# Kernel optimization log

Measured on AMD Instinct MI355X. Metric: run time of the kernel, lower is better.

## Reference

```python
import jax, jax.numpy as jnp
import numpy as np

TRIM = 0.2
ALPHA = 0.5
SCALES = 4
B, H, W = 64, 384, 512


def _normalize_robust(x, mask):
    # per-sample masked median shift, masked mean-abs-dev scale (MiDaS SSI norm)
    b = x.shape[0]
    xf = x.reshape(b, -1)
    mf = mask.reshape(b, -1)
    n = mf.sum(axis=1)                                   # valid count per row
    s = jnp.sort(jnp.where(mf, xf, jnp.inf), axis=1)     # masked-out -> +inf, sorted to tail
    med_idx = jnp.maximum((n - 1) // 2, 0)               # torch.median = lower median
    shift = jnp.take_along_axis(s, med_idx[:, None], axis=1)      # [b,1]
    scale = (jnp.abs(xf - shift) * mf).sum(axis=1) / n.astype(xf.dtype)
    return ((xf - shift) / scale[:, None]).reshape(x.shape)


def _gradient_loss(pred, targ):
    mask = targ > 0
    gx = jnp.abs(pred[:, :, 1:] - pred[:, :, :-1])
    gy = jnp.abs(pred[:, 1:, :] - pred[:, :-1, :])
    mx = (mask[:, :, 1:] & mask[:, :, :-1]).astype(pred.dtype)
    my = (mask[:, 1:, :] & mask[:, :-1, :]).astype(pred.dtype)
    norm = mask.sum(axis=(1, 2))
    loss = (gx * mx).sum(axis=(1, 2)) + (gy * my).sum(axis=(1, 2))
    valid = norm > 0
    loss = jnp.where(valid, loss / jnp.maximum(norm, 1).astype(pred.dtype), 0.0)
    return loss.mean()


def _multiscale_gradient_loss(pred, targ):
    total = jnp.asarray(0.0, pred.dtype)
    for scale in range(SCALES):
        step = 2 ** scale
        total = total + _gradient_loss(pred[:, ::step, ::step], targ[:, ::step, ::step])
    return total


def _trimmed_mae(pred, targ):
    b = pred.shape[0]
    p = pred.reshape(b, -1)
    t = targ.reshape(b, -1)
    n_px = p.shape[1]
    mask = t > 0
    res = jnp.where(mask, jnp.abs(p - t), 0.0)
    # NOTE: faithful to source, which indexes the UNSORTED res at max_index
    # (sorted_res is computed then never used for the threshold).
    max_index = (~mask).sum(axis=1) + int((1.0 - TRIM) * n_px)
    max_index = jnp.minimum(max_index, n_px - 1)
    thr = jnp.take_along_axis(res, max_index[:, None], axis=1)    # [b,1]
    res = jnp.where(res > thr, 0.0, res)
    norm = 2 * mask.sum(axis=1)
    valid = norm > 0
    loss = res.sum(axis=1)
    loss = jnp.where(valid, loss / jnp.maximum(norm, 1).astype(p.dtype), 0.0)
    return loss.mean()


def setup_inputs() -> dict:
    key = jax.random.key(0)
    kp, kt = jax.random.split(key)
    prediction = jax.random.normal(kp, (B, H, W), dtype=jnp.float32)
    target = jax.random.normal(kt, (B, H, W), dtype=jnp.float32)
    return {"prediction": prediction, "target": target}


def reference(prediction, target):
    mask = target > 0
    pred_n = _normalize_robust(prediction, mask)
    targ_n = _normalize_robust(target, mask)
    loss = _trimmed_mae(pred_n, targ_n)
    loss = loss + ALPHA * _multiscale_gradient_loss(pred_n, targ_n)
    return loss
```

## Files before the change

kernel.cpp:

```cpp
#include <hip/hip_runtime.h>
#include <stdint.h>

#define B 64
#define H 384
#define W 512
#define NPX (H*W)
#define TRIM_IDX 157286
#define RPW 8

#define NBA 2048
#define CAPW 256
#define NSLOT 64
#define CAPD 12288
#define SCAP 6144
#define DELTA 0.03f

#define N_OFF    0
#define MS_OFF   64
#define TS_OFF   256
#define GS_OFF   320
#define TSUM_OFF 576
#define SB_OFF   704
#define CB_OFF   832
#define OVF_OFF  960
#define ZERO_U32 1088
#define BL_OFF   1088
#define BH_OFF   1216
#define K_OFF    1344
#define EQ_OFF   1472
#define SH_OFF   1600
#define RS_OFF   1728
#define THR_OFF  1856
#define C2_OFF   1920
#define CNTW_OFF 1984
#define FIX_U32  (1984 + 2*B*NSLOT)
#define BUF_OFF  FIX_U32

__device__ __forceinline__ uint32_t fmap(float f) {
    uint32_t b = __float_as_uint(f);
    return (b & 0x80000000u) ? ~b : (b | 0x80000000u);
}
__device__ __forceinline__ float funmap(uint32_t u) {
    uint32_t b = (u & 0x80000000u) ? (u & 0x7fffffffu) : ~u;
    return __uint_as_float(b);
}

__global__ void __launch_bounds__(1024) sample_kernel(const float* __restrict__ pred,
                                                      const float* __restrict__ targ,
                                                      uint32_t* __restrict__ ws) {
    __shared__ uint32_t kp[SCAP], kt[SCAP];
    __shared__ uint32_t h[4096];
    __shared__ uint32_t sc[256];
    __shared__ uint32_t s_ct, s_lo12, s_hi12, s_clo, s_bl, s_bh;
    const int b = blockIdx.x;
    const int t = threadIdx.x;
    const int lane = t & 63;
    if (t == 0) s_ct = 0;
    __syncthreads();
    const float4* pb = (const float4*)(pred + (size_t)b * NPX);
    const float4* tb = (const float4*)(targ + (size_t)b * NPX);
    #pragma unroll
    for (int c = 0; c < 2; c++) {
        int j = t + c * 1024;
        int q = ((j >> 6) * 1536) + (j & 63);
        float4 tv = tb[q], pv = pb[q];
        float tA[4] = {tv.x, tv.y, tv.z, tv.w};
        float pA[4] = {pv.x, pv.y, pv.z, pv.w};
        #pragma unroll
        for (int e = 0; e < 4; e++) {
            bool msk = tA[e] > 0.f;
            unsigned long long bal = __ballot(msk);
            if (bal) {
                int leader = __ffsll((long long)bal) - 1;
                uint32_t base = 0;
                if (lane == leader) base = atomicAdd(&s_ct, (uint32_t)__popcll(bal));
                base = (uint32_t)__shfl((int)base, leader, 64);
                if (msk) {
                    uint32_t off = base + (uint32_t)__popcll(bal & ((1ull << lane) - 1ull));
                    if (off < SCAP) { kt[off] = fmap(tA[e]); kp[off] = fmap(pA[e]); }
                }
            }
        }
    }
    __syncthreads();
    const uint32_t ct = s_ct;
    const bool ok = (ct > 0) && (ct <= SCAP);
    for (int w = 0; w < 2; w++) {
        const uint32_t* K = (w == 0) ? kp : kt;
        uint32_t BL = 0, BH = 0xFFFFFu;
        if (ok) {
            uint32_t rlo = (uint32_t)((0.5f - DELTA) * (float)ct);
            uint32_t rhi = (uint32_t)((0.5f + DELTA) * (float)ct);
            if (rhi >= ct) rhi = ct - 1;
            for (int i = t; i < 4096; i += 1024) h[i] = 0;
            __syncthreads();
            for (uint32_t j = t; j < ct; j += 1024) atomicAdd(&h[K[j] >> 20], 1u);
            __syncthreads();
            uint32_t ms = 0;
            if (t < 256) { for (int i = 0; i < 16; i++) ms += h[t * 16 + i]; sc[t] = ms; }
            __syncthreads();
            for (int off = 1; off < 256; off <<= 1) {
                uint32_t a = (t < 256 && t >= off) ? sc[t - off] : 0u;
                __syncthreads();
                if (t < 256) sc[t] += a;
                __syncthreads();
            }
            if (t < 256) {
                uint32_t incl = sc[t], excl = incl - ms;
                if (rlo >= excl && rlo < incl) {
                    uint32_t c2 = excl;
                    for (int i = 0; i < 16; i++) {
                        uint32_t hv = h[t * 16 + i];
                        if (rlo < c2 + hv) { s_lo12 = t * 16 + i; s_clo = c2; break; }
                        c2 += hv;
                    }
                }
                if (rhi >= excl && rhi < incl) {
                    uint32_t c2 = excl;
                    for (int i = 0; i < 16; i++) {
                        uint32_t hv = h[t * 16 + i];
                        if (rhi < c2 + hv) { s_hi12 = t * 16 + i; break; }
                        c2 += hv;
                    }
                }
            }
            __syncthreads();
            const uint32_t lo12 = s_lo12, hi12 = s_hi12, clo = s_clo;
            const uint32_t range = (hi12 - lo12 + 1) << 8;
            if (range > 4096) {
                BL = lo12 << 8; BH = (hi12 << 8) | 255u;
            } else {
                for (int i = t; i < 4096; i += 1024) h[i] = 0;
                __syncthreads();
                const uint32_t base20 = lo12 << 8;
                for (uint32_t j = t; j < ct; j += 1024) {
                    uint32_t u = K[j], u12 = u >> 20;
                    if (u12 >= lo12 && u12 <= hi12) atomicAdd(&h[(u >> 12) - base20], 1u);
                }
                __syncthreads();
                const uint32_t r2lo = rlo - clo, r2hi = rhi - clo;
                uint32_t ms2 = 0;
                if (t < 256) { for (int i = 0; i < 16; i++) ms2 += h[t * 16 + i]; sc[t] = ms2; }
                __syncthreads();
                for (int off = 1; off < 256; off <<= 1) {
                    uint32_t a = (t < 256 && t >= off) ? sc[t - off] : 0u;
                    __syncthreads();
                    if (t < 256) sc[t] += a;
                    __syncthreads();
                }
                if (t < 256) {
                    uint32_t incl = sc[t], excl = incl - ms2;
                    if (r2lo >= excl && r2lo < incl) {
                        uint32_t c2 = excl;
                        for (int i = 0; i < 16; i++) {
                            uint32_t hv = h[t * 16 + i];
                            if (r2lo < c2 + hv) { s_bl = base20 + t * 16 + i; break; }
                            c2 += hv;
                        }
                    }
                    if (r2hi >= excl && r2hi < incl) {
                        uint32_t c2 = excl;
                        for (int i = 0; i < 16; i++) {
                            uint32_t hv = h[t * 16 + i];
                            if (r2hi < c2 + hv) { s_bh = base20 + t * 16 + i; break; }
                            c2 += hv;
                        }
                    }
                }
                __syncthreads();
                BL = s_bl; BH = s_bh;
            }
        }
        if (t == 0) { ws[BL_OFF + w * B + b] = BL; ws[BH_OFF + w * B + b] = BH; }
        __syncthreads();
    }
}

__global__ void __launch_bounds__(256) collect_kernel(const float* __restrict__ pred,
                                                      const float* __restrict__ targ,
                                                      uint32_t* __restrict__ ws, int capw) {
    const int b = blockIdx.y;
    const int t = threadIdx.x;
    const int lane = t & 63;
    const int slot = (blockIdx.x << 2) + (t >> 6);
    const uint32_t BLp = ws[BL_OFF + b],     BHp = ws[BH_OFF + b];
    const uint32_t BLt = ws[BL_OFF + B + b], BHt = ws[BH_OFF + B + b];
    const float4* pb = (const float4*)(pred + (size_t)b * NPX);
    const float4* tb = (const float4*)(targ + (size_t)b * NPX);
    const int tid = blockIdx.x * 256 + t;
    float* bufp = ((float*)(ws + BUF_OFF)) + ((size_t)b * NSLOT + slot) * capw;
    float* buft = ((float*)(ws + BUF_OFF)) + (((size_t)B + b) * NSLOT + slot) * capw;
    float sbp = 0.f, sbt = 0.f, sump = 0.f, sumt = 0.f;
    uint32_t nloc = 0, cbp = 0, cbt = 0;
    uint32_t wp = 0, wt = 0;
    #pragma unroll
    for (int r = 0; r < 3; r++) {
        float4 ta0 = tb[tid + (4*r+0)*4096], ta1 = tb[tid + (4*r+1)*4096];
        float4 ta2 = tb[tid + (4*r+2)*4096], ta3 = tb[tid + (4*r+3)*4096];
        float4 pa0 = pb[tid + (4*r+0)*4096], pa1 = pb[tid + (4*r+1)*4096];
        float4 pa2 = pb[tid + (4*r+2)*4096], pa3 = pb[tid + (4*r+3)*4096];
        float tA[16] = {ta0.x,ta0.y,ta0.z,ta0.w, ta1.x,ta1.y,ta1.z,ta1.w,
                        ta2.x,ta2.y,ta2.z,ta2.w, ta3.x,ta3.y,ta3.z,ta3.w};
        float pA[16] = {pa0.x,pa0.y,pa0.z,pa0.w, pa1.x,pa1.y,pa1.z,pa1.w,
                        pa2.x,pa2.y,pa2.z,pa2.w, pa3.x,pa3.y,pa3.z,pa3.w};
        uint32_t mbp = 0, mbt = 0;
        #pragma unroll
        for (int e = 0; e < 16; e++) {
            float tv = tA[e], pv = pA[e];
            if (tv > 0.f) {
                nloc++; sumt += tv; sump += pv;
                uint32_t up = fmap(pv) >> 12, ut = fmap(tv) >> 12;
                if (up < BLp) { cbp++; sbp += pv; }
                else if (up <= BHp) mbp |= (1u << e);
                if (ut < BLt) { cbt++; sbt += tv; }
                else if (ut <= BHt) mbt |= (1u << e);
            }
        }
        uint32_t packed = (uint32_t)__popc(mbp) | ((uint32_t)__popc(mbt) << 16);
        uint32_t scan = packed;
        #pragma unroll
        for (int off = 1; off < 64; off <<= 1) {
            uint32_t v = (uint32_t)__shfl_up((int)scan, off, 64);
            if (lane >= off) scan += v;
        }
        uint32_t tot = (uint32_t)__shfl((int)scan, 63, 64);
        uint32_t exl = scan - packed;
        uint32_t op = wp + (exl & 0xFFFFu);
        uint32_t ot = wt + (exl >> 16);
        if (mbp | mbt) {
            #pragma unroll
            for (int e = 0; e < 16; e++) {
                if ((mbp >> e) & 1u) { if (op < (uint32_t)capw) bufp[op] = pA[e]; op++; }
                if ((mbt >> e) & 1u) { if (ot < (uint32_t)capw) buft[ot] = tA[e]; ot++; }
            }
        }
        wp += tot & 0xFFFFu;
        wt += tot >> 16;
    }
    if (lane == 0) {
        ws[CNTW_OFF + b * NSLOT + slot] = wp;
        ws[CNTW_OFF + (B + b) * NSLOT + slot] = wt;
        if (wp > (uint32_t)capw) ws[OVF_OFF + b] = 1u;
        if (wt > (uint32_t)capw) ws[OVF_OFF + B + b] = 1u;
    }
    for (int off = 32; off; off >>= 1) {
        nloc += __shfl_down(nloc, off, 64);
        sump += __shfl_down(sump, off, 64);
        sumt += __shfl_down(sumt, off, 64);
        sbp  += __shfl_down(sbp, off, 64);
        sbt  += __shfl_down(sbt, off, 64);
        cbp  += __shfl_down(cbp, off, 64);
        cbt  += __shfl_down(cbt, off, 64);
    }
    if (lane == 0) {
        if (nloc) atomicAdd(ws + N_OFF + b, nloc);
        atomicAdd(((float*)(ws + TSUM_OFF)) + b, sump);
        atomicAdd(((float*)(ws + TSUM_OFF)) + B + b, sumt);
        atomicAdd(((float*)(ws + SB_OFF)) + b, sbp);
        atomicAdd(((float*)(ws + SB_OFF)) + B + b, sbt);
        if (cbp) atomicAdd(ws + CB_OFF + b, cbp);
        if (cbt) atomicAdd(ws + CB_OFF + B + b, cbt);
    }
}

__global__ void small3_kernel(const float* __restrict__ pred,
                              const float* __restrict__ targ,
                              uint32_t* __restrict__ ws, int capw) {
    const int b = blockIdx.x, which = blockIdx.y;
    const int t = threadIdx.x;
    __shared__ float dense[CAPD];
    __shared__ uint32_t cnt[4096];
    __shared__ float fsm[4096];
    __shared__ uint32_t sc[256];
    __shared__ float sfl[256];
    __shared__ uint32_t scnt[NSLOT], soff[NSLOT];
    __shared__ uint32_t r_bin, r_k, s_Ctot;
    __shared__ float r_f, s_facc;
    const uint32_t n = ws[N_OFF + b];
    const uint32_t k0 = (n - 1u) >> 1;
    const uint32_t CBv = ws[CB_OFF + which * B + b];
    const uint32_t* cw = ws + CNTW_OFF + (which * B + b) * NSLOT;
    const float* bufb = ((const float*)(ws + BUF_OFF)) + ((size_t)which * B + b) * NSLOT * capw;
    const float* Tp = targ + (size_t)b * NPX;
    const float* Pp = pred + (size_t)b * NPX;

    uint32_t myc = (t < NSLOT) ? cw[t] : 0u;
    sc[t] = myc;
    __syncthreads();
    for (int off = 1; off < NSLOT; off <<= 1) {
        uint32_t a = (t >= off) ? sc[t - off] : 0u;
        __syncthreads();
        sc[t] += a;
        __syncthreads();
    }
    if (t < NSLOT) { scnt[t] = myc; soff[t] = sc[t] - myc; }
    if (t == NSLOT - 1) s_Ctot = sc[t];
    __syncthreads();
    const uint32_t Ctot = s_Ctot;
    const long k_in = (long)k0 - (long)CBv;
    const bool fast = (capw > 0) && (ws[OVF_OFF + which * B + b] == 0u) &&
                      (Ctot <= (uint32_t)CAPD) && (k_in >= 0) && (k_in < (long)Ctot);
    if (fast) {
        const int s = t >> 2;
        const float* sb_ = bufb + (size_t)s * capw;
        const uint32_t nn = scnt[s], o = soff[s];
        for (uint32_t j = (uint32_t)(t & 3); j < nn; j += 4) dense[o + j] = sb_[j];
    }
    __syncthreads();

    uint32_t kr = fast ? (uint32_t)k_in : k0;

    for (int i = t; i < 4096; i += 256) { cnt[i] = 0; fsm[i] = 0.f; }
    __syncthreads();
    if (fast) {
        for (uint32_t j = t; j < Ctot; j += 256) {
            float v = dense[j];
            uint32_t key = fmap(v) >> 20;
            atomicAdd(&cnt[key], 1u); atomicAdd(&fsm[key], v);
        }
    } else {
        for (int j = t; j < NPX; j += 256) {
            float tvv = Tp[j];
            if (tvv > 0.f) {
                float v = (which == 0) ? Pp[j] : tvv;
                uint32_t key = fmap(v) >> 20;
                atomicAdd(&cnt[key], 1u); atomicAdd(&fsm[key], v);
            }
        }
    }
    __syncthreads();
    {
        uint32_t ms = 0; float mf = 0.f;
        #pragma unroll
        for (int i = 0; i < 16; i++) { ms += cnt[t * 16 + i]; mf += fsm[t * 16 + i]; }
        sc[t] = ms; sfl[t] = mf;
        __syncthreads();
        for (int off = 1; off < 256; off <<= 1) {
            uint32_t a = (t >= off) ? sc[t - off] : 0u;
            float af = (t >= off) ? sfl[t - off] : 0.f;
            __syncthreads();
            sc[t] += a; sfl[t] += af;
            __syncthreads();
        }
        uint32_t incl = sc[t], excl = incl - ms;
        float fx = sfl[t] - mf;
        if (kr >= excl && kr < incl) {
            uint32_t c = excl, bin = 0, nk = 0; float f = fx;
            for (int i = 0; i < 16; i++) {
                uint32_t hv = cnt[t * 16 + i];
                if (kr < c + hv) { bin = t * 16 + i; nk = kr - c; break; }
                c += hv; f += fsm[t * 16 + i];
            }
            r_bin = bin; r_k = nk; r_f = f;
        }
    }
    __syncthreads();
    const uint32_t sel0 = r_bin;
    kr = r_k;
    if (t == 0) s_facc = r_f;
    __syncthreads();

    for (int i = t; i < NBA; i += 256) { cnt[i] = 0; fsm[i] = 0.f; }
    __syncthreads();
    if (fast) {
        for (uint32_t j = t; j < Ctot; j += 256) {
            float v = dense[j];
            uint32_t u = fmap(v);
            if ((u >> 20) == sel0) {
                uint32_t key = (u >> 9) & (NBA - 1u);
                atomicAdd(&cnt[key], 1u); atomicAdd(&fsm[key], v);
            }
        }
    } else {
        for (int j = t; j < NPX; j += 256) {
            float tvv = Tp[j];
            if (tvv > 0.f) {
                float v = (which == 0) ? Pp[j] : tvv;
                uint32_t u = fmap(v);
                if ((u >> 20) == sel0) {
                    uint32_t key = (u >> 9) & (NBA - 1u);
                    atomicAdd(&cnt[key], 1u); atomicAdd(&fsm[key], v);
                }
            }
        }
    }
    __syncthreads();
    {
        uint32_t ms = 0; float mf = 0.f;
        #pragma unroll
        for (int i = 0; i < 8; i++) { ms += cnt[t * 8 + i]; mf += fsm[t * 8 + i]; }
        sc[t] = ms; sfl[t] = mf;
        __syncthreads();
        for (int off = 1; off < 256; off <<= 1) {
            uint32_t a = (t >= off) ? sc[t - off] : 0u;
            float af = (t >= off) ? sfl[t - off] : 0.f;
            __syncthreads();
            sc[t] += a; sfl[t] += af;
            __syncthreads();
        }
        uint32_t incl = sc[t], excl = incl - ms;
        float fx = sfl[t] - mf;
        if (kr >= excl && kr < incl) {
            uint32_t c = excl, bin = 0, nk = 0; float f = fx;
            for (int i = 0; i < 8; i++) {
                uint32_t hv = cnt[t * 8 + i];
                if (kr < c + hv) { bin = t * 8 + i; nk = kr - c; break; }
                c += hv; f += fsm[t * 8 + i];
            }
            r_bin = bin; r_k = nk; r_f = f;
        }
    }
    __syncthreads();
    const uint32_t pfx23 = (sel0 << 11) | r_bin;
    kr = r_k;
    if (t == 0) s_facc += r_f;
    __syncthreads();

    for (int i = t; i < 512; i += 256) { cnt[i] = 0; fsm[i] = 0.f; }
    __syncthreads();
    if (fast) {
        for (uint32_t j = t; j < Ctot; j += 256) {
            float v = dense[j];
            uint32_t u = fmap(v);
            if ((u >> 9) == pfx23) {
                uint32_t key = u & 511u;
                atomicAdd(&cnt[key], 1u); atomicAdd(&fsm[key], v);
            }
        }
    } else {
        for (int j = t; j < NPX; j += 256) {
            float tvv = Tp[j];
            if (tvv > 0.f) {
                float v = (which == 0) ? Pp[j] : tvv;
                uint32_t u = fmap(v);
                if ((u >> 9) == pfx23) {
                    uint32_t key = u & 511u;
                    atomicAdd(&cnt[key], 1u); atomicAdd(&fsm[key], v);
                }
            }
        }
    }
    __syncthreads();
    {
        uint32_t ms = 0; float mf = 0.f;
        #pragma unroll
        for (int i = 0; i < 2; i++) { ms += cnt[t * 2 + i]; mf += fsm[t * 2 + i]; }
        sc[t] = ms; sfl[t] = mf;
        __syncthreads();
        for (int off = 1; off < 256; off <<= 1) {
            uint32_t a = (t >= off) ? sc[t - off] : 0u;
            float af = (t >= off) ? sfl[t - off] : 0.f;
            __syncthreads();
            sc[t] += a; sfl[t] += af;
            __syncthreads();
        }
        uint32_t incl = sc[t], excl = incl - ms;
        float fx = sfl[t] - mf;
        if (kr >= excl && kr < incl) {
            uint32_t c = excl, bin = 0, nk = 0, e = 0; float f = fx;
            for (int i = 0; i < 2; i++) {
                uint32_t hv = cnt[t * 2 + i];
                if (kr < c + hv) { bin = t * 2 + i; nk = kr - c; e = hv; break; }
                c += hv; f += fsm[t * 2 + i];
            }
            uint32_t u = (pfx23 << 9) | bin;
            ((float*)(ws + SH_OFF))[which * B + b] = funmap(u);
            ws[K_OFF + which * B + b] = nk;
            ws[EQ_OFF + which * B + b] = e;
            float* sb = ((float*)(ws + SB_OFF)) + which * B + b;
            float below = s_facc + f;
            *sb = fast ? (*sb + below) : below;
        }
    }
}

__global__ void param_kernel(const float* __restrict__ pred,
                             const float* __restrict__ targ,
                             uint32_t* __restrict__ ws) {
    const int b = threadIdx.x;
    if (b >= B) return;
    const uint32_t n = ws[N_OFF + b];
    const uint32_t k0 = (n - 1u) >> 1;
    float med[2], rs[2];
    uint32_t nab[2];
    #pragma unroll
    for (int w = 0; w < 2; w++) {
        float m = ((const float*)(ws + SH_OFF))[w * B + b];
        uint32_t k3 = ws[K_OFF + w * B + b];
        uint32_t e = ws[EQ_OFF + w * B + b];
        float SBv = ((const float*)(ws + SB_OFF))[w * B + b];
        float ST = ((const float*)(ws + TSUM_OFF))[w * B + b];
        uint32_t CB = k0 - k3;
        uint32_t na = n - CB - e;
        float Sab = ST - SBv - (float)e * m;
        float absdev = (Sab - (float)na * m) + ((float)CB * m - SBv);
        float scale = absdev / (float)n;
        med[w] = m; nab[w] = na;
        rs[w] = 1.f / scale;
        ((float*)(ws + RS_OFF))[w * B + b] = rs[w];
    }
    uint32_t c2 = nab[1];
    ws[C2_OFF + b] = c2;
    uint32_t mi = (uint32_t)NPX - c2 + (uint32_t)TRIM_IDX;
    if (mi > (uint32_t)(NPX - 1)) mi = NPX - 1;
    float p = pred[(size_t)b * NPX + mi];
    float t = targ[(size_t)b * NPX + mi];
    float pn = (p - med[0]) * rs[0], tn = (t - med[1]) * rs[1];
    ((float*)(ws + THR_OFF))[b] = (tn > 0.f) ? fabsf(pn - tn) : 0.f;
}

__global__ void __launch_bounds__(256) loss_kernel(const float* __restrict__ pred,
                                                   const float* __restrict__ targ,
                                                   uint32_t* __restrict__ ws) {
    const int wid = (blockIdx.x << 2) + (threadIdx.x >> 6);
    const int b = wid / (H / RPW);
    const int s0 = (wid - b * (H / RPW)) * RPW;
    const int l = threadIdx.x & 63;
    const int col = l << 3;
    const float sp = ((const float*)(ws + SH_OFF))[b];
    const float st = ((const float*)(ws + SH_OFF))[B + b];
    const float rp = ((const float*)(ws + RS_OFF))[b];
    const float rt = ((const float*)(ws + RS_OFF))[B + b];
    const float thr = ((const float*)(ws + THR_OFF))[b];
    const float* Pp = pred + (size_t)b * NPX;
    const float* Tp = targ + (size_t)b * NPX;

    const bool g1 = s0 >= 1, g2 = s0 >= 2, g4 = s0 >= 4, g8 = s0 >= 8;
    float rT[2][8], rPN[2][8];
    {
        const int roA = (g1 ? (s0 - 1) : s0) * W + col;
        const int roB = (g2 ? (s0 - 2) : s0) * W + col;
        float4 a0 = *(const float4*)(Tp + roA), a1 = *(const float4*)(Tp + roA + 4);
        float4 b0 = *(const float4*)(Pp + roA), b1 = *(const float4*)(Pp + roA + 4);
        float4 c0 = *(const float4*)(Tp + roB), c1 = *(const float4*)(Tp + roB + 4);
        float4 d0 = *(const float4*)(Pp + roB), d1 = *(const float4*)(Pp + roB + 4);
        float ta[8] = {a0.x,a0.y,a0.z,a0.w,a1.x,a1.y,a1.z,a1.w};
        float pa[8] = {b0.x,b0.y,b0.z,b0.w,b1.x,b1.y,b1.z,b1.w};
        float tc[8] = {c0.x,c0.y,c0.z,c0.w,c1.x,c1.y,c1.z,c1.w};
        float pc[8] = {d0.x,d0.y,d0.z,d0.w,d1.x,d1.y,d1.z,d1.w};
        #pragma unroll
        for (int k = 0; k < 8; k++) {
            rT[1][k] = ta[k]; rPN[1][k] = (pa[k] - sp) * rp;
            rT[0][k] = tc[k]; rPN[0][k] = (pc[k] - sp) * rp;
        }
    }

    float tl = 0.f, gl0 = 0.f, gl1 = 0.f, gl2 = 0.f, gl3 = 0.f;
    uint32_t mc = 0;

    #pragma unroll
    for (int it = 0; it < RPW; ++it) {
        const int ro = (s0 + it) * W + col;
        const int cur = it & 1, prv = cur ^ 1;
        float4 a0 = *(const float4*)(Tp + ro), a1 = *(const float4*)(Tp + ro + 4);
        float4 b0 = *(const float4*)(Pp + ro), b1 = *(const float4*)(Pp + ro + 4);
        float t[8] = {a0.x,a0.y,a0.z,a0.w,a1.x,a1.y,a1.z,a1.w};
        float p[8] = {b0.x,b0.y,b0.z,b0.w,b1.x,b1.y,b1.z,b1.w};
        float t4a = 0.f, t4b = 0.f, p4a = 0.f, p4b = 0.f, t8a = 0.f, p8a = 0.f;
        if (it == 0) {
            const int ro4 = g4 ? ro - 4 * W : ro;
            t4a = Tp[ro4]; t4b = Tp[ro4 + 4]; p4a = Pp[ro4]; p4b = Pp[ro4 + 4];
            const int ro8 = g8 ? ro - 8 * W : ro;
            t8a = Tp[ro8]; p8a = Pp[ro8];
        }
        if (it == 4) {
            const int ro4 = ro - 4 * W;
            t4a = Tp[ro4]; t4b = Tp[ro4 + 4]; p4a = Pp[ro4]; p4b = Pp[ro4 + 4];
        }
        float pn[8]; bool m[8];
        #pragma unroll
        for (int k = 0; k < 8; k++) { pn[k] = (p[k] - sp) * rp; m[k] = t[k] > st; }

        #pragma unroll
        for (int k = 0; k < 8; k++) {
            if (m[k]) {
                float tn = (t[k] - st) * rt;
                float r = fabsf(pn[k] - tn);
                if (r <= thr) tl += r;
            }
        }
        float t7p = __shfl_up(t[7], 1), pn7p = __shfl_up(pn[7], 1);
        if (l > 0 && m[0] && t7p > st) gl0 += fabsf(pn[0] - pn7p);
        #pragma unroll
        for (int k = 1; k < 8; k++) if (m[k] && m[k - 1]) gl0 += fabsf(pn[k] - pn[k - 1]);
        if (it > 0 || g1) {
            #pragma unroll
            for (int k = 0; k < 8; k++)
                if (m[k] && rT[prv][k] > st) gl0 += fabsf(pn[k] - rPN[prv][k]);
        }
        if ((it & 1) == 0) {
            float t6p = __shfl_up(t[6], 1), pn6p = __shfl_up(pn[6], 1);
            mc += (uint32_t)m[0] + m[2] + m[4] + m[6];
            if (l > 0 && m[0] && t6p > st) gl1 += fabsf(pn[0] - pn6p);
            if (m[2] && m[0]) gl1 += fabsf(pn[2] - pn[0]);
            if (m[4] && m[2]) gl1 += fabsf(pn[4] - pn[2]);
            if (m[6] && m[4]) gl1 += fabsf(pn[6] - pn[4]);
            if (it >= 2 || g2) {
                if (m[0] && rT[cur][0] > st) gl1 += fabsf(pn[0] - rPN[cur][0]);
                if (m[2] && rT[cur][2] > st) gl1 += fabsf(pn[2] - rPN[cur][2]);
                if (m[4] && rT[cur][4] > st) gl1 += fabsf(pn[4] - rPN[cur][4]);
                if (m[6] && rT[cur][6] > st) gl1 += fabsf(pn[6] - rPN[cur][6]);
            }
            if ((it & 3) == 0) {
                float t4p = __shfl_up(t[4], 1), pn4p = __shfl_up(pn[4], 1);
                mc += ((uint32_t)m[0] + m[4]) << 11;
                if (l > 0 && m[0] && t4p > st) gl2 += fabsf(pn[0] - pn4p);
                if (m[4] && m[0]) gl2 += fabsf(pn[4] - pn[0]);
                if (it == 4 || g4) {
                    if (m[0] && t4a > st) gl2 += fabsf(pn[0] - (p4a - sp) * rp);
                    if (m[4] && t4b > st) gl2 += fabsf(pn[4] - (p4b - sp) * rp);
                }
                if (it == 0) {
                    float t0p = __shfl_up(t[0], 1), pn0p = __shfl_up(pn[0], 1);
                    mc += ((uint32_t)m[0]) << 22;
                    if (l > 0 && m[0] && t0p > st) gl3 += fabsf(pn[0] - pn0p);
                    if (g8 && m[0] && t8a > st) gl3 += fabsf(pn[0] - (p8a - sp) * rp);
                }
            }
        }
        #pragma unroll
        for (int k = 0; k < 8; k++) { rT[cur][k] = t[k]; rPN[cur][k] = pn[k]; }
    }

    for (int off = 32; off; off >>= 1) {
        tl  += __shfl_down(tl, off, 64);
        gl0 += __shfl_down(gl0, off, 64);
        gl1 += __shfl_down(gl1, off, 64);
        gl2 += __shfl_down(gl2, off, 64);
        gl3 += __shfl_down(gl3, off, 64);
        mc  += __shfl_down(mc, off, 64);
    }
    if (l == 0) {
        float* gs = (float*)(ws + GS_OFF);
        atomicAdd(((float*)(ws + TS_OFF)) + b, tl);
        atomicAdd(gs + b, gl0);
        atomicAdd(gs + B + b, gl1);
        atomicAdd(gs + 2 * B + b, gl2);
        atomicAdd(gs + 3 * B + b, gl3);
        atomicAdd(ws + MS_OFF + b, mc & 0x7FFu);
        atomicAdd(ws + MS_OFF + B + b, (mc >> 11) & 0x7FFu);
        atomicAdd(ws + MS_OFF + 2 * B + b, mc >> 22);
    }
}

__global__ void finalize_kernel(const uint32_t* __restrict__ ws, float* __restrict__ out) {
    const int b = threadIdx.x;
    float v = 0.f;
    if (b < B) {
        float c2 = (float)ws[C2_OFF + b];
        const float* tsum = (const float*)(ws + TS_OFF);
        const float* gsum = (const float*)(ws + GS_OFF);
        float tm = (c2 > 0.f) ? tsum[b] / (2.f * c2) : 0.f;
        float g = (c2 > 0.f) ? gsum[b] / c2 : 0.f;
        for (int z = 0; z < 3; z++) {
            float ms = (float)ws[MS_OFF + z * B + b];
            g += (ms > 0.f) ? gsum[(1 + z) * B + b] / ms : 0.f;
        }
        v = tm + 0.5f * g;
    }
    for (int off = 32; off; off >>= 1) v += __shfl_down(v, off, 64);
    if (b == 0) out[0] = v * (1.f / 64.f);
}

extern "C" void kernel_launch(void* const* d_in, const int* in_sizes, int n_in,
                              void* d_out, int out_size, void* d_ws, size_t ws_size,
                              hipStream_t stream) {
    const float* pred = (const float*)d_in[0];
    const float* targ = (const float*)d_in[1];
    float* out = (float*)d_out;
    uint32_t* ws = (uint32_t*)d_ws;

    long avail = (long)(ws_size / 4) - (long)FIX_U32;
    int capw = 0;
    if (avail > 0) {
        long c = avail / (2L * B * NSLOT);
        capw = (int)(c < CAPW ? c : CAPW);
    }

    hipMemsetAsync(ws, 0, (size_t)ZERO_U32 * 4, stream);

    sample_kernel<<<dim3(B), 1024, 0, stream>>>(pred, targ, ws);
    collect_kernel<<<dim3(16, B), 256, 0, stream>>>(pred, targ, ws, capw);
    small3_kernel<<<dim3(B, 2), 256, 0, stream>>>(pred, targ, ws, capw);
    param_kernel<<<1, 64, 0, stream>>>(pred, targ, ws);
    loss_kernel<<<dim3(B * (H / RPW) / 4), 256, 0, stream>>>(pred, targ, ws);
    finalize_kernel<<<1, 64, 0, stream>>>(ws, out);
}
```

Baseline: 146.0 us.

## Remove memset and param kernel launches, fold params into loss kernel

Drops the workspace memset by zeroing the per-sample accumulators inside sample_kernel, and removes param_kernel by having each loss_kernel thread recompute median, scale and trim threshold from the workspace. It also changes collect_kernel so each block reads a contiguous chunk instead of a strided one. Together these remove two stream operations and improve locality. In exchange every loss thread does redundant scalar math plus a gather load for the threshold.

```diff
diff --git a/kernel.cpp b/kernel.cpp
--- a/kernel.cpp
+++ b/kernel.cpp
@@ -23,13 +23,11 @@
 #define SB_OFF   704
 #define CB_OFF   832
 #define OVF_OFF  960
-#define ZERO_U32 1088
 #define BL_OFF   1088
 #define BH_OFF   1216
 #define K_OFF    1344
 #define EQ_OFF   1472
 #define SH_OFF   1600
-#define RS_OFF   1728
 #define THR_OFF  1856
 #define C2_OFF   1920
 #define CNTW_OFF 1984
@@ -55,7 +53,21 @@
     const int b = blockIdx.x;
     const int t = threadIdx.x;
     const int lane = t & 63;
-    if (t == 0) s_ct = 0;
+    if (t == 0) {
+        s_ct = 0;
+        ws[N_OFF + b] = 0; ws[TS_OFF + b] = 0;
+        #pragma unroll
+        for (int z = 0; z < 3; z++) ws[MS_OFF + z * B + b] = 0;
+        #pragma unroll
+        for (int w2 = 0; w2 < 4; w2++) ws[GS_OFF + w2 * B + b] = 0;
+        #pragma unroll
+        for (int w2 = 0; w2 < 2; w2++) {
+            ws[TSUM_OFF + w2 * B + b] = 0;
+            ws[SB_OFF + w2 * B + b] = 0;
+            ws[CB_OFF + w2 * B + b] = 0;
+            ws[OVF_OFF + w2 * B + b] = 0;
+        }
+    }
     __syncthreads();
     const float4* pb = (const float4*)(pred + (size_t)b * NPX);
     const float4* tb = (const float4*)(targ + (size_t)b * NPX);
@@ -187,7 +199,7 @@
     const uint32_t BLt = ws[BL_OFF + B + b], BHt = ws[BH_OFF + B + b];
     const float4* pb = (const float4*)(pred + (size_t)b * NPX);
     const float4* tb = (const float4*)(targ + (size_t)b * NPX);
-    const int tid = blockIdx.x * 256 + t;
+    const int bbase = blockIdx.x * 3072;
     float* bufp = ((float*)(ws + BUF_OFF)) + ((size_t)b * NSLOT + slot) * capw;
     float* buft = ((float*)(ws + BUF_OFF)) + (((size_t)B + b) * NSLOT + slot) * capw;
     float sbp = 0.f, sbt = 0.f, sump = 0.f, sumt = 0.f;
@@ -195,10 +207,9 @@
     uint32_t wp = 0, wt = 0;
     #pragma unroll
     for (int r = 0; r < 3; r++) {
-        float4 ta0 = tb[tid + (4*r+0)*4096], ta1 = tb[tid + (4*r+1)*4096];
-        float4 ta2 = tb[tid + (4*r+2)*4096], ta3 = tb[tid + (4*r+3)*4096];
-        float4 pa0 = pb[tid + (4*r+0)*4096], pa1 = pb[tid + (4*r+1)*4096];
-        float4 pa2 = pb[tid + (4*r+2)*4096], pa3 = pb[tid + (4*r+3)*4096];
+        const int rb = bbase + (4 * r) * 256 + t;
+        float4 ta0 = tb[rb], ta1 = tb[rb + 256], ta2 = tb[rb + 512], ta3 = tb[rb + 768];
+        float4 pa0 = pb[rb], pa1 = pb[rb + 256], pa2 = pb[rb + 512], pa3 = pb[rb + 768];
         float tA[16] = {ta0.x,ta0.y,ta0.z,ta0.w, ta1.x,ta1.y,ta1.z,ta1.w,
                         ta2.x,ta2.y,ta2.z,ta2.w, ta3.x,ta3.y,ta3.z,ta3.w};
         float pA[16] = {pa0.x,pa0.y,pa0.z,pa0.w, pa1.x,pa1.y,pa1.z,pa1.w,
@@ -474,14 +485,20 @@
     }
 }
 
-__global__ void param_kernel(const float* __restrict__ pred,
-                             const float* __restrict__ targ,
-                             uint32_t* __restrict__ ws) {
-    const int b = threadIdx.x;
-    if (b >= B) return;
+__global__ void __launch_bounds__(256) loss_kernel(const float* __restrict__ pred,
+                                                   const float* __restrict__ targ,
+                                                   uint32_t* __restrict__ ws) {
+    const int wid = (blockIdx.x << 2) + (threadIdx.x >> 6);
+    const int b = wid / (H / RPW);
+    const int s0 = (wid - b * (H / RPW)) * RPW;
+    const int l = threadIdx.x & 63;
+    const int col = l << 3;
+    const float* Pp = pred + (size_t)b * NPX;
+    const float* Tp = targ + (size_t)b * NPX;
+
     const uint32_t n = ws[N_OFF + b];
     const uint32_t k0 = (n - 1u) >> 1;
-    float med[2], rs[2];
+    float med[2], rsv[2];
     uint32_t nab[2];
     #pragma unroll
     for (int w = 0; w < 2; w++) {
@@ -496,34 +513,19 @@
         float absdev = (Sab - (float)na * m) + ((float)CB * m - SBv);
         float scale = absdev / (float)n;
         med[w] = m; nab[w] = na;
-        rs[w] = 1.f / scale;
-        ((float*)(ws + RS_OFF))[w * B + b] = rs[w];
-    }
-    uint32_t c2 = nab[1];
-    ws[C2_OFF + b] = c2;
-    uint32_t mi = (uint32_t)NPX - c2 + (uint32_t)TRIM_IDX;
+        rsv[w] = 1.f / scale;
+    }
+    const uint32_t c2u = nab[1];
+    if (threadIdx.x == 0) ws[C2_OFF + b] = c2u;
+    uint32_t mi = (uint32_t)NPX - c2u + (uint32_t)TRIM_IDX;
     if (mi > (uint32_t)(NPX - 1)) mi = NPX - 1;
-    float p = pred[(size_t)b * NPX + mi];
-    float t = targ[(size_t)b * NPX + mi];
-    float pn = (p - med[0]) * rs[0], tn = (t - med[1]) * rs[1];
-    ((float*)(ws + THR_OFF))[b] = (tn > 0.f) ? fabsf(pn - tn) : 0.f;
-}
-
-__global__ void __launch_bounds__(256) loss_kernel(const float* __restrict__ pred,
-                                                   const float* __restrict__ targ,
-                                                   uint32_t* __restrict__ ws) {
-    const int wid = (blockIdx.x << 2) + (threadIdx.x >> 6);
-    const int b = wid / (H / RPW);
-    const int s0 = (wid - b * (H / RPW)) * RPW;
-    const int l = threadIdx.x & 63;
-    const int col = l << 3;
-    const float sp = ((const float*)(ws + SH_OFF))[b];
-    const float st = ((const float*)(ws + SH_OFF))[B + b];
-    const float rp = ((const float*)(ws + RS_OFF))[b];
-    const float rt = ((const float*)(ws + RS_OFF))[B + b];
-    const float thr = ((const float*)(ws + THR_OFF))[b];
-    const float* Pp = pred + (size_t)b * NPX;
-    const float* Tp = targ + (size_t)b * NPX;
+    const float sp = med[0], st = med[1], rp = rsv[0], rt = rsv[1];
+    float thr;
+    {
+        float p = Pp[mi], t = Tp[mi];
+        float pn_ = (p - sp) * rp, tn_ = (t - st) * rt;
+        thr = (tn_ > 0.f) ? fabsf(pn_ - tn_) : 0.f;
+    }
 
     const bool g1 = s0 >= 1, g2 = s0 >= 2, g4 = s0 >= 4, g8 = s0 >= 8;
     float rT[2][8], rPN[2][8];
@@ -677,12 +679,9 @@
         capw = (int)(c < CAPW ? c : CAPW);
     }
 
-    hipMemsetAsync(ws, 0, (size_t)ZERO_U32 * 4, stream);
-
     sample_kernel<<<dim3(B), 1024, 0, stream>>>(pred, targ, ws);
     collect_kernel<<<dim3(16, B), 256, 0, stream>>>(pred, targ, ws, capw);
     small3_kernel<<<dim3(B, 2), 256, 0, stream>>>(pred, targ, ws, capw);
-    param_kernel<<<1, 64, 0, stream>>>(pred, targ, ws);
     loss_kernel<<<dim3(B * (H / RPW) / 4), 256, 0, stream>>>(pred, targ, ws);
     finalize_kernel<<<1, 64, 0, stream>>>(ws, out);
 }
```

New measurement: 139.3 us. -4.5%, faster.
